# Optimization experiments

Hardware: AMD Instinct MI355X
Metric: run time of the kernel (lower is better)

Reference implementation:

```python
import jax, jax.numpy as jnp
import numpy as np

D_MODEL = 1024
NUM_HEADS = 16
DEPTH = D_MODEL // NUM_HEADS


def setup_inputs() -> dict:
    key = jax.random.key(0)
    ks = jax.random.split(key, 11)
    B, S = 2, 2048
    scale = 1.0 / np.sqrt(D_MODEL)
    inp = {
        "q": jax.random.normal(ks[0], (B, S, D_MODEL), dtype=jnp.float32),
        "k": jax.random.normal(ks[1], (B, S, D_MODEL), dtype=jnp.float32),
        "v": jax.random.normal(ks[2], (B, S, D_MODEL), dtype=jnp.float32),
        "mask": jnp.zeros((B, 1, 1, S), dtype=jnp.float32),
        "wq": jax.random.normal(ks[3], (D_MODEL, D_MODEL), dtype=jnp.float32) * scale,
        "bq": jnp.zeros((D_MODEL,), dtype=jnp.float32),
        "wk": jax.random.normal(ks[4], (D_MODEL, D_MODEL), dtype=jnp.float32) * scale,
        "bk": jnp.zeros((D_MODEL,), dtype=jnp.float32),
        "wv": jax.random.normal(ks[5], (D_MODEL, D_MODEL), dtype=jnp.float32) * scale,
        "bv": jnp.zeros((D_MODEL,), dtype=jnp.float32),
        "wo": jax.random.normal(ks[6], (D_MODEL, D_MODEL), dtype=jnp.float32) * scale,
        "bo": jnp.zeros((D_MODEL,), dtype=jnp.float32),
    }
    return inp


def _split_heads(x):
    # [B, S, D] -> [B, H, S, depth]
    B, S, _ = x.shape
    return x.reshape(B, S, NUM_HEADS, DEPTH).transpose(0, 2, 1, 3)


def reference(q, k, v, mask, wq, bq, wk, bk, wv, bv, wo, bo):
    B, S, _ = q.shape
    qh = _split_heads(q @ wq + bq)  # [B,H,S,d]
    kh = _split_heads(k @ wk + bk)
    vh = _split_heads(v @ wv + bv)
    logits = jnp.einsum("bhsd,bhtd->bhst", qh, kh) / jnp.sqrt(
        jnp.asarray(DEPTH, dtype=qh.dtype)
    )
    logits = logits + mask * -1e9
    attn = jax.nn.softmax(logits, axis=-1)  # [B,H,S,S]
    ctx = jnp.einsum("bhst,bhtd->bhsd", attn, vh)
    ctx = ctx.transpose(0, 2, 1, 3).reshape(B, S, D_MODEL)
    out = ctx @ wo + bo
    return out, attn
```

## Files before the change

kernel.cpp:

```cpp
#include <hip/hip_runtime.h>
#include <cstdint>
#include <cstddef>

typedef __bf16 bf16;
typedef __attribute__((ext_vector_type(8))) __bf16 bf16x8;
typedef __attribute__((ext_vector_type(4))) __bf16 bf16x4;
typedef __attribute__((ext_vector_type(4))) float f32x4;

#define DM 1024
#define NH 16
#define DEPTH 64
#define SEQ 2048
#define NB 2

__device__ __forceinline__ void split2(float x, bf16& h, bf16& l) {
    h = (bf16)x;
    l = (bf16)(x - (float)h);
}

__device__ __forceinline__ f32x4 mfma16(bf16x8 a, bf16x8 b, f32x4 c) {
    return __builtin_amdgcn_mfma_f32_16x16x32_bf16(a, b, c, 0, 0, 0);
}

__global__ __launch_bounds__(256) void split_kernel(const float* __restrict__ x,
                                                    bf16* __restrict__ hi,
                                                    bf16* __restrict__ lo, int n) {
    int i = (blockIdx.x * 256 + threadIdx.x) * 4;
    if (i >= n) return;
    float4 v = *(const float4*)(x + i);
    bf16 h0, l0, h1, l1, h2, l2, h3, l3;
    split2(v.x, h0, l0); split2(v.y, h1, l1);
    split2(v.z, h2, l2); split2(v.w, h3, l3);
    bf16x4 hv = {h0, h1, h2, h3}, lv = {l0, l1, l2, l3};
    *(bf16x4*)(hi + i) = hv;
    *(bf16x4*)(lo + i) = lv;
}

__global__ __launch_bounds__(256) void wsplit_t(const float* __restrict__ w,
                                                bf16* __restrict__ hi,
                                                bf16* __restrict__ lo) {
    __shared__ float tile[64][65];
    int t = threadIdx.x;
    int c0 = blockIdx.x * 64;
    int r0 = blockIdx.y * 64;
    int r = t >> 2, cg = (t & 3) * 16;
#pragma unroll
    for (int j = 0; j < 16; j += 4) {
        float4 v = *(const float4*)(w + (size_t)(r0 + r) * DM + c0 + cg + j);
        tile[r][cg + j] = v.x; tile[r][cg + j + 1] = v.y;
        tile[r][cg + j + 2] = v.z; tile[r][cg + j + 3] = v.w;
    }
    __syncthreads();
    int n = t >> 2, kg = (t & 3) * 16;
    bf16x8 hv0, hv1, lv0, lv1;
#pragma unroll
    for (int i = 0; i < 8; i++) {
        bf16 h, l;
        split2(tile[kg + i][n], h, l); hv0[i] = h; lv0[i] = l;
        split2(tile[kg + 8 + i][n], h, l); hv1[i] = h; lv1[i] = l;
    }
    size_t o = (size_t)(c0 + n) * DM + r0 + kg;
    *(bf16x8*)(hi + o) = hv0; *(bf16x8*)(hi + o + 8) = hv1;
    *(bf16x8*)(lo + o) = lv0; *(bf16x8*)(lo + o + 8) = lv1;
}

__global__ __launch_bounds__(256) void gemm_split(
    const bf16* __restrict__ Ah, const bf16* __restrict__ Al,
    const bf16* __restrict__ Bh, const bf16* __restrict__ Bl,
    const float* __restrict__ bias,
    bf16* __restrict__ Ch, bf16* __restrict__ Cl, float* __restrict__ Cf) {
    __shared__ bf16 lAh[128][40], lAl[128][40], lBh[128][40], lBl[128][40];
    int t = threadIdx.x;
    int m0 = blockIdx.x * 128, n0 = blockIdx.y * 128;
    int l = t & 63, w = t >> 6;
    int quad = l >> 4, ln = l & 15;
    int mr = (w & 1) * 64, nr = (w >> 1) * 64;

    f32x4 acc[4][4];
#pragma unroll
    for (int r = 0; r < 4; r++)
#pragma unroll
        for (int c = 0; c < 4; c++) acc[r][c] = (f32x4){0.f, 0.f, 0.f, 0.f};

    int srow = t >> 1, shalf = (t & 1) * 16;
    for (int kk = 0; kk < DM / 32; kk++) {
        int k0 = kk * 32;
        size_t ga = (size_t)(m0 + srow) * DM + k0 + shalf;
        size_t gb = (size_t)(n0 + srow) * DM + k0 + shalf;
        *(bf16x8*)&lAh[srow][shalf]     = *(const bf16x8*)(Ah + ga);
        *(bf16x8*)&lAh[srow][shalf + 8] = *(const bf16x8*)(Ah + ga + 8);
        *(bf16x8*)&lAl[srow][shalf]     = *(const bf16x8*)(Al + ga);
        *(bf16x8*)&lAl[srow][shalf + 8] = *(const bf16x8*)(Al + ga + 8);
        *(bf16x8*)&lBh[srow][shalf]     = *(const bf16x8*)(Bh + gb);
        *(bf16x8*)&lBh[srow][shalf + 8] = *(const bf16x8*)(Bh + gb + 8);
        *(bf16x8*)&lBl[srow][shalf]     = *(const bf16x8*)(Bl + gb);
        *(bf16x8*)&lBl[srow][shalf + 8] = *(const bf16x8*)(Bl + gb + 8);
        __syncthreads();

        bf16x8 af_h[4], af_l[4], bf_h[4], bf_l[4];
#pragma unroll
        for (int r = 0; r < 4; r++) {
            af_h[r] = *(const bf16x8*)&lAh[mr + r * 16 + ln][quad * 8];
            af_l[r] = *(const bf16x8*)&lAl[mr + r * 16 + ln][quad * 8];
        }
#pragma unroll
        for (int c = 0; c < 4; c++) {
            bf_h[c] = *(const bf16x8*)&lBh[nr + c * 16 + ln][quad * 8];
            bf_l[c] = *(const bf16x8*)&lBl[nr + c * 16 + ln][quad * 8];
        }
#pragma unroll
        for (int r = 0; r < 4; r++)
#pragma unroll
            for (int c = 0; c < 4; c++) {
                acc[r][c] = mfma16(af_h[r], bf_h[c], acc[r][c]);
                acc[r][c] = mfma16(af_h[r], bf_l[c], acc[r][c]);
                acc[r][c] = mfma16(af_l[r], bf_h[c], acc[r][c]);
            }
        __syncthreads();
    }

#pragma unroll
    for (int c = 0; c < 4; c++) {
        int col = n0 + nr + c * 16 + ln;
        float bv = bias[col];
#pragma unroll
        for (int r = 0; r < 4; r++) {
            int rowb = m0 + mr + r * 16 + quad * 4;
#pragma unroll
            for (int i = 0; i < 4; i++) {
                float v = acc[r][c][i] + bv;
                size_t o = (size_t)(rowb + i) * DM + col;
                if (Cf) {
                    Cf[o] = v;
                } else {
                    bf16 h, lo_;
                    split2(v, h, lo_);
                    Ch[o] = h; Cl[o] = lo_;
                }
            }
        }
    }
}

__global__ __launch_bounds__(256) void vtrans(const bf16* __restrict__ vh_h,
                                              const bf16* __restrict__ vh_l,
                                              bf16* __restrict__ vt_h,
                                              bf16* __restrict__ vt_l) {
    __shared__ bf16 tile[64][72];
    int t = threadIdx.x;
    int s0 = blockIdx.x * 64;
    int bh = blockIdx.y;
    int b = bh >> 4, h = bh & 15;
    const bf16* src[2] = {vh_h, vh_l};
    bf16* dst[2] = {vt_h, vt_l};
#pragma unroll
    for (int p = 0; p < 2; p++) {
#pragma unroll
        for (int rnd = 0; rnd < 2; rnd++) {
            int unit = t + rnd * 256;
            int r = unit >> 3, cg = (unit & 7) * 8;
            *(bf16x8*)&tile[r][cg] =
                *(const bf16x8*)(src[p] + (size_t)(b * SEQ + s0 + r) * DM + h * DEPTH + cg);
        }
        __syncthreads();
#pragma unroll
        for (int rnd = 0; rnd < 2; rnd++) {
            int unit = t + rnd * 256;
            int d = unit >> 3, sg = (unit & 7) * 8;
            bf16x8 v;
#pragma unroll
            for (int j = 0; j < 8; j++) v[j] = tile[sg + j][d];
            *(bf16x8*)(dst[p] + (size_t)(bh * DEPTH + d) * SEQ + s0 + sg) = v;
        }
        __syncthreads();
    }
}

__global__ __launch_bounds__(256) void attn_kernel(
    const bf16* __restrict__ qh_h, const bf16* __restrict__ qh_l,
    const bf16* __restrict__ kh_h, const bf16* __restrict__ kh_l,
    const bf16* __restrict__ vt_h, const bf16* __restrict__ vt_l,
    const float* __restrict__ mask,
    float* __restrict__ attn, bf16* __restrict__ ctx_h, bf16* __restrict__ ctx_l) {
    __shared__ bf16 lQh[64][72], lQl[64][72], lKh[64][72], lKl[64][72];
    __shared__ bf16 lVh[64][72], lVl[64][72], lPh[64][72], lPl[64][72];
    int t = threadIdx.x;
    int m0 = blockIdx.x * 64;
    int bh = blockIdx.y;
    int b = bh >> 4, h = bh & 15;
    int l = t & 63, w = t >> 6, quad = l >> 4, ln = l & 15;
    int mr = w * 16;

#pragma unroll
    for (int rnd = 0; rnd < 2; rnd++) {
        int unit = t + rnd * 256;
        int r = unit >> 3, cg = (unit & 7) * 8;
        size_t g = (size_t)(b * SEQ + m0 + r) * DM + h * DEPTH + cg;
        *(bf16x8*)&lQh[r][cg] = *(const bf16x8*)(qh_h + g);
        *(bf16x8*)&lQl[r][cg] = *(const bf16x8*)(qh_l + g);
    }
    __syncthreads();
    bf16x8 qf_h[2], qf_l[2];
#pragma unroll
    for (int kk = 0; kk < 2; kk++) {
        qf_h[kk] = *(const bf16x8*)&lQh[mr + ln][kk * 32 + quad * 8];
        qf_l[kk] = *(const bf16x8*)&lQl[mr + ln][kk * 32 + quad * 8];
    }

    float rowsum[4] = {0.f, 0.f, 0.f, 0.f};
    for (int ct = 0; ct < SEQ / 64; ct++) {
        int t0 = ct * 64;
#pragma unroll
        for (int rnd = 0; rnd < 2; rnd++) {
            int unit = t + rnd * 256;
            int r = unit >> 3, cg = (unit & 7) * 8;
            size_t g = (size_t)(b * SEQ + t0 + r) * DM + h * DEPTH + cg;
            *(bf16x8*)&lKh[r][cg] = *(const bf16x8*)(kh_h + g);
            *(bf16x8*)&lKl[r][cg] = *(const bf16x8*)(kh_l + g);
        }
        __syncthreads();
#pragma unroll
        for (int c = 0; c < 4; c++) {
            f32x4 s = (f32x4){0.f, 0.f, 0.f, 0.f};
#pragma unroll
            for (int kk = 0; kk < 2; kk++) {
                bf16x8 kb_h = *(const bf16x8*)&lKh[c * 16 + ln][kk * 32 + quad * 8];
                bf16x8 kb_l = *(const bf16x8*)&lKl[c * 16 + ln][kk * 32 + quad * 8];
                s = mfma16(qf_h[kk], kb_h, s);
                s = mfma16(qf_h[kk], kb_l, s);
                s = mfma16(qf_l[kk], kb_h, s);
            }
            int col = t0 + c * 16 + ln;
            float mv = mask[b * SEQ + col] * -1e9f;
#pragma unroll
            for (int i = 0; i < 4; i++) rowsum[i] += __expf(s[i] * 0.125f + mv);
        }
        __syncthreads();
    }
#pragma unroll
    for (int m = 1; m < 16; m <<= 1)
#pragma unroll
        for (int i = 0; i < 4; i++) rowsum[i] += __shfl_xor(rowsum[i], m, 64);
    float linv[4];
#pragma unroll
    for (int i = 0; i < 4; i++) linv[i] = 1.0f / rowsum[i];

    f32x4 o[4];
#pragma unroll
    for (int c = 0; c < 4; c++) o[c] = (f32x4){0.f, 0.f, 0.f, 0.f};

    for (int ct = 0; ct < SEQ / 64; ct++) {
        int t0 = ct * 64;
#pragma unroll
        for (int rnd = 0; rnd < 2; rnd++) {
            int unit = t + rnd * 256;
            int r = unit >> 3, cg = (unit & 7) * 8;
            size_t g = (size_t)(b * SEQ + t0 + r) * DM + h * DEPTH + cg;
            *(bf16x8*)&lKh[r][cg] = *(const bf16x8*)(kh_h + g);
            *(bf16x8*)&lKl[r][cg] = *(const bf16x8*)(kh_l + g);
            size_t gv = (size_t)(bh * DEPTH + r) * SEQ + t0 + cg;
            *(bf16x8*)&lVh[r][cg] = *(const bf16x8*)(vt_h + gv);
            *(bf16x8*)&lVl[r][cg] = *(const bf16x8*)(vt_l + gv);
        }
        __syncthreads();
#pragma unroll
        for (int c = 0; c < 4; c++) {
            f32x4 s = (f32x4){0.f, 0.f, 0.f, 0.f};
#pragma unroll
            for (int kk = 0; kk < 2; kk++) {
                bf16x8 kb_h = *(const bf16x8*)&lKh[c * 16 + ln][kk * 32 + quad * 8];
                bf16x8 kb_l = *(const bf16x8*)&lKl[c * 16 + ln][kk * 32 + quad * 8];
                s = mfma16(qf_h[kk], kb_h, s);
                s = mfma16(qf_h[kk], kb_l, s);
                s = mfma16(qf_l[kk], kb_h, s);
            }
            int col = t0 + c * 16 + ln;
            float mv = mask[b * SEQ + col] * -1e9f;
#pragma unroll
            for (int i = 0; i < 4; i++) {
                float p = __expf(s[i] * 0.125f + mv) * linv[i];
                attn[((size_t)bh * SEQ + m0 + mr + quad * 4 + i) * SEQ + col] = p;
                bf16 ph, pl;
                split2(p, ph, pl);
                lPh[mr + quad * 4 + i][c * 16 + ln] = ph;
                lPl[mr + quad * 4 + i][c * 16 + ln] = pl;
            }
        }
        __syncthreads();
#pragma unroll
        for (int kk = 0; kk < 2; kk++) {
            bf16x8 pa_h = *(const bf16x8*)&lPh[mr + ln][kk * 32 + quad * 8];
            bf16x8 pa_l = *(const bf16x8*)&lPl[mr + ln][kk * 32 + quad * 8];
#pragma unroll
            for (int c2 = 0; c2 < 4; c2++) {
                bf16x8 vb_h = *(const bf16x8*)&lVh[c2 * 16 + ln][kk * 32 + quad * 8];
                bf16x8 vb_l = *(const bf16x8*)&lVl[c2 * 16 + ln][kk * 32 + quad * 8];
                o[c2] = mfma16(pa_h, vb_h, o[c2]);
                o[c2] = mfma16(pa_h, vb_l, o[c2]);
                o[c2] = mfma16(pa_l, vb_h, o[c2]);
            }
        }
        __syncthreads();
    }

#pragma unroll
    for (int c2 = 0; c2 < 4; c2++) {
        int d = c2 * 16 + ln;
#pragma unroll
        for (int i = 0; i < 4; i++) {
            int row = m0 + mr + quad * 4 + i;
            bf16 hh, ll;
            split2(o[c2][i], hh, ll);
            size_t oo = (size_t)(b * SEQ + row) * DM + h * DEPTH + d;
            ctx_h[oo] = hh; ctx_l[oo] = ll;
        }
    }
}

extern "C" void kernel_launch(void* const* d_in, const int* in_sizes, int n_in,
                              void* d_out, int out_size, void* d_ws, size_t ws_size,
                              hipStream_t stream) {
    (void)in_sizes; (void)n_in; (void)out_size; (void)ws_size;
    const float* q    = (const float*)d_in[0];
    const float* k    = (const float*)d_in[1];
    const float* v    = (const float*)d_in[2];
    const float* mask = (const float*)d_in[3];
    const float* wq   = (const float*)d_in[4];
    const float* bq   = (const float*)d_in[5];
    const float* wk   = (const float*)d_in[6];
    const float* bk   = (const float*)d_in[7];
    const float* wv   = (const float*)d_in[8];
    const float* bv   = (const float*)d_in[9];
    const float* wo   = (const float*)d_in[10];
    const float* bo   = (const float*)d_in[11];

    float* out  = (float*)d_out;
    float* attn = out + (size_t)NB * SEQ * DM;

    const size_t E  = (size_t)NB * SEQ * DM;
    const size_t WE = (size_t)DM * DM;

    bf16* p = (bf16*)d_ws;
    bf16* q_h = p;            bf16* q_l = q_h + E;
    bf16* k_h = q_l + E;      bf16* k_l = k_h + E;
    bf16* v_h = k_l + E;      bf16* v_l = v_h + E;
    bf16* wqT_h = v_l + E;    bf16* wqT_l = wqT_h + WE;
    bf16* wkT_h = wqT_l + WE; bf16* wkT_l = wkT_h + WE;
    bf16* wvT_h = wkT_l + WE; bf16* wvT_l = wvT_h + WE;
    bf16* woT_h = wvT_l + WE; bf16* woT_l = woT_h + WE;
    bf16* qh_h = woT_l + WE;  bf16* qh_l = qh_h + E;
    bf16* kh_h = qh_l + E;    bf16* kh_l = kh_h + E;
    bf16* vh_h = kh_l + E;    bf16* vh_l = vh_h + E;
    bf16* vt_h = q_h;  bf16* vt_l = q_l;
    bf16* ctx_h = k_h; bf16* ctx_l = k_l;

    dim3 blk(256);
    split_kernel<<<(int)(E / 1024), blk, 0, stream>>>(q, q_h, q_l, (int)E);
    split_kernel<<<(int)(E / 1024), blk, 0, stream>>>(k, k_h, k_l, (int)E);
    split_kernel<<<(int)(E / 1024), blk, 0, stream>>>(v, v_h, v_l, (int)E);
    wsplit_t<<<dim3(16, 16), blk, 0, stream>>>(wq, wqT_h, wqT_l);
    wsplit_t<<<dim3(16, 16), blk, 0, stream>>>(wk, wkT_h, wkT_l);
    wsplit_t<<<dim3(16, 16), blk, 0, stream>>>(wv, wvT_h, wvT_l);
    wsplit_t<<<dim3(16, 16), blk, 0, stream>>>(wo, woT_h, woT_l);

    gemm_split<<<dim3(32, 8), blk, 0, stream>>>(q_h, q_l, wqT_h, wqT_l, bq, qh_h, qh_l, nullptr);
    gemm_split<<<dim3(32, 8), blk, 0, stream>>>(k_h, k_l, wkT_h, wkT_l, bk, kh_h, kh_l, nullptr);
    gemm_split<<<dim3(32, 8), blk, 0, stream>>>(v_h, v_l, wvT_h, wvT_l, bv, vh_h, vh_l, nullptr);

    vtrans<<<dim3(32, 32), blk, 0, stream>>>(vh_h, vh_l, vt_h, vt_l);

    attn_kernel<<<dim3(32, 32), blk, 0, stream>>>(qh_h, qh_l, kh_h, kh_l, vt_h, vt_l,
                                                  mask, attn, ctx_h, ctx_l);

    gemm_split<<<dim3(32, 8), blk, 0, stream>>>(ctx_h, ctx_l, woT_h, woT_l, bo,
                                                nullptr, nullptr, out);
}
```

Before: 1.031 ms.

## Double-buffer GEMM and attention tiles with direct global-to-LDS loads and swizzling

```diff
diff --git a/kernel.cpp b/kernel.cpp
--- a/kernel.cpp
+++ b/kernel.cpp
@@ -20,6 +20,12 @@
 
 __device__ __forceinline__ f32x4 mfma16(bf16x8 a, bf16x8 b, f32x4 c) {
     return __builtin_amdgcn_mfma_f32_16x16x32_bf16(a, b, c, 0, 0, 0);
+}
+
+__device__ __forceinline__ void gload16(const bf16* g, bf16* s) {
+    __builtin_amdgcn_global_load_lds(
+        (const __attribute__((address_space(1))) void*)g,
+        (__attribute__((address_space(3))) void*)s, 16, 0, 0);
 }
 
 __global__ __launch_bounds__(256) void split_kernel(const float* __restrict__ x,
@@ -64,68 +70,82 @@
     *(bf16x8*)(lo + o) = lv0; *(bf16x8*)(lo + o + 8) = lv1;
 }
 
-__global__ __launch_bounds__(256) void gemm_split(
+__global__ __launch_bounds__(512) void gemm_split(
     const bf16* __restrict__ Ah, const bf16* __restrict__ Al,
     const bf16* __restrict__ Bh, const bf16* __restrict__ Bl,
     const float* __restrict__ bias,
     bf16* __restrict__ Ch, bf16* __restrict__ Cl, float* __restrict__ Cf) {
-    __shared__ bf16 lAh[128][40], lAl[128][40], lBh[128][40], lBl[128][40];
+    __shared__ bf16 lds4[2][4][128 * 64];
     int t = threadIdx.x;
     int m0 = blockIdx.x * 128, n0 = blockIdx.y * 128;
     int l = t & 63, w = t >> 6;
     int quad = l >> 4, ln = l & 15;
-    int mr = (w & 1) * 64, nr = (w >> 1) * 64;
-
-    f32x4 acc[4][4];
+    int wr = w >> 2, wc = w & 3;
+    int rch = l >> 3, c16 = l & 7;
+    int sx0 = (quad ^ (ln & 7)) << 3;
+
+    int bufid = w >> 1;
+    const bf16* src = (bufid == 0) ? Ah : (bufid == 1) ? Al : (bufid == 2) ? Bh : Bl;
+    int rbase = (bufid < 2) ? m0 : n0;
+    int ch0 = (w & 1) * 8;
+
+    auto stage = [&](int db, int k0) {
+#pragma unroll
+        for (int j = 0; j < 8; j++) {
+            int chunk = ch0 + j;
+            int row = chunk * 8 + rch;
+            gload16(src + (size_t)(rbase + row) * DM + k0 + ((c16 ^ (row & 7)) << 3),
+                    &lds4[db][bufid][chunk * 512]);
+        }
+    };
+
+    f32x4 acc[4][2];
 #pragma unroll
     for (int r = 0; r < 4; r++)
 #pragma unroll
-        for (int c = 0; c < 4; c++) acc[r][c] = (f32x4){0.f, 0.f, 0.f, 0.f};
-
-    int srow = t >> 1, shalf = (t & 1) * 16;
-    for (int kk = 0; kk < DM / 32; kk++) {
-        int k0 = kk * 32;
-        size_t ga = (size_t)(m0 + srow) * DM + k0 + shalf;
-        size_t gb = (size_t)(n0 + srow) * DM + k0 + shalf;
-        *(bf16x8*)&lAh[srow][shalf]     = *(const bf16x8*)(Ah + ga);
-        *(bf16x8*)&lAh[srow][shalf + 8] = *(const bf16x8*)(Ah + ga + 8);
-        *(bf16x8*)&lAl[srow][shalf]     = *(const bf16x8*)(Al + ga);
-        *(bf16x8*)&lAl[srow][shalf + 8] = *(const bf16x8*)(Al + ga + 8);
-        *(bf16x8*)&lBh[srow][shalf]     = *(const bf16x8*)(Bh + gb);
-        *(bf16x8*)&lBh[srow][shalf + 8] = *(const bf16x8*)(Bh + gb + 8);
-        *(bf16x8*)&lBl[srow][shalf]     = *(const bf16x8*)(Bl + gb);
-        *(bf16x8*)&lBl[srow][shalf + 8] = *(const bf16x8*)(Bl + gb + 8);
+        for (int c = 0; c < 2; c++) acc[r][c] = (f32x4){0.f, 0.f, 0.f, 0.f};
+
+    stage(0, 0);
+    __syncthreads();
+
+    for (int kk = 0; kk < DM / 64; kk++) {
+        int cur = kk & 1;
+        if (kk < DM / 64 - 1) stage(cur ^ 1, (kk + 1) * 64);
+#pragma unroll
+        for (int k2 = 0; k2 < 2; k2++) {
+            int so = sx0 ^ (k2 << 5);
+            bf16x8 ah[4], al[4], bh[2], bl[2];
+#pragma unroll
+            for (int r = 0; r < 4; r++) {
+                int ro = (wr * 64 + r * 16 + ln) << 6;
+                ah[r] = *(const bf16x8*)&lds4[cur][0][ro + so];
+                al[r] = *(const bf16x8*)&lds4[cur][1][ro + so];
+            }
+#pragma unroll
+            for (int c = 0; c < 2; c++) {
+                int ro = (wc * 32 + c * 16 + ln) << 6;
+                bh[c] = *(const bf16x8*)&lds4[cur][2][ro + so];
+                bl[c] = *(const bf16x8*)&lds4[cur][3][ro + so];
+            }
+#pragma unroll
+            for (int r = 0; r < 4; r++)
+#pragma unroll
+                for (int c = 0; c < 2; c++) {
+                    acc[r][c] = mfma16(ah[r], bh[c], acc[r][c]);
+                    acc[r][c] = mfma16(ah[r], bl[c], acc[r][c]);
+                    acc[r][c] = mfma16(al[r], bh[c], acc[r][c]);
+                }
+        }
         __syncthreads();
-
-        bf16x8 af_h[4], af_l[4], bf_h[4], bf_l[4];
+    }
+
+#pragma unroll
+    for (int c = 0; c < 2; c++) {
+        int col = n0 + wc * 32 + c * 16 + ln;
+        float bv = bias[col];
 #pragma unroll
         for (int r = 0; r < 4; r++) {
-            af_h[r] = *(const bf16x8*)&lAh[mr + r * 16 + ln][quad * 8];
-            af_l[r] = *(const bf16x8*)&lAl[mr + r * 16 + ln][quad * 8];
-        }
-#pragma unroll
-        for (int c = 0; c < 4; c++) {
-            bf_h[c] = *(const bf16x8*)&lBh[nr + c * 16 + ln][quad * 8];
-            bf_l[c] = *(const bf16x8*)&lBl[nr + c * 16 + ln][quad * 8];
-        }
-#pragma unroll
-        for (int r = 0; r < 4; r++)
-#pragma unroll
-            for (int c = 0; c < 4; c++) {
-                acc[r][c] = mfma16(af_h[r], bf_h[c], acc[r][c]);
-                acc[r][c] = mfma16(af_h[r], bf_l[c], acc[r][c]);
-                acc[r][c] = mfma16(af_l[r], bf_h[c], acc[r][c]);
-            }
-        __syncthreads();
-    }
-
-#pragma unroll
-    for (int c = 0; c < 4; c++) {
-        int col = n0 + nr + c * 16 + ln;
-        float bv = bias[col];
-#pragma unroll
-        for (int r = 0; r < 4; r++) {
-            int rowb = m0 + mr + r * 16 + quad * 4;
+            int rowb = m0 + wr * 64 + r * 16 + quad * 4;
 #pragma unroll
             for (int i = 0; i < 4; i++) {
                 float v = acc[r][c][i] + bv;
@@ -176,56 +196,79 @@
     }
 }
 
-__global__ __launch_bounds__(256) void attn_kernel(
+#define PST 76
+__global__ __launch_bounds__(512) void attn_kernel(
     const bf16* __restrict__ qh_h, const bf16* __restrict__ qh_l,
     const bf16* __restrict__ kh_h, const bf16* __restrict__ kh_l,
     const bf16* __restrict__ vt_h, const bf16* __restrict__ vt_l,
     const float* __restrict__ mask,
     float* __restrict__ attn, bf16* __restrict__ ctx_h, bf16* __restrict__ ctx_l) {
-    __shared__ bf16 lQh[64][72], lQl[64][72], lKh[64][72], lKl[64][72];
-    __shared__ bf16 lVh[64][72], lVl[64][72], lPh[64][72], lPl[64][72];
+    __shared__ bf16 lK[2][2][64 * 64];
+    __shared__ bf16 lV[2][2][64 * 64];
+    __shared__ bf16 lPh[128 * PST], lPl[128 * PST];
     int t = threadIdx.x;
-    int m0 = blockIdx.x * 64;
+    int m0 = blockIdx.x * 128;
     int bh = blockIdx.y;
     int b = bh >> 4, h = bh & 15;
     int l = t & 63, w = t >> 6, quad = l >> 4, ln = l & 15;
-    int mr = w * 16;
-
-#pragma unroll
-    for (int rnd = 0; rnd < 2; rnd++) {
-        int unit = t + rnd * 256;
-        int r = unit >> 3, cg = (unit & 7) * 8;
-        size_t g = (size_t)(b * SEQ + m0 + r) * DM + h * DEPTH + cg;
-        *(bf16x8*)&lQh[r][cg] = *(const bf16x8*)(qh_h + g);
-        *(bf16x8*)&lQl[r][cg] = *(const bf16x8*)(qh_l + g);
-    }
+    int rch = l >> 3, c16 = l & 7;
+    int sx0 = (quad ^ (ln & 7)) << 3;
+
+    bf16x8 qf_h[2], qf_l[2];
+    {
+        size_t qrow = (size_t)(b * SEQ + m0 + w * 16 + ln) * DM + h * DEPTH;
+#pragma unroll
+        for (int kk = 0; kk < 2; kk++) {
+            qf_h[kk] = *(const bf16x8*)(qh_h + qrow + kk * 32 + quad * 8);
+            qf_l[kk] = *(const bf16x8*)(qh_l + qrow + kk * 32 + quad * 8);
+        }
+    }
+
+    const bf16* ksrc1 = (w < 4) ? kh_h : kh_l;
+    int kbuf1 = (w < 4) ? 0 : 1;
+    int kch0 = (w & 3) * 2;
+    auto stageK = [&](int db, int t0) {
+#pragma unroll
+        for (int j = 0; j < 2; j++) {
+            int chunk = kch0 + j;
+            int row = chunk * 8 + rch;
+            gload16(ksrc1 + (size_t)(b * SEQ + t0 + row) * DM + h * DEPTH +
+                        ((c16 ^ (row & 7)) << 3),
+                    &lK[db][kbuf1][chunk * 512]);
+        }
+    };
+    int tgt = w >> 1;
+    const bf16* ksrc2 = (tgt == 0) ? kh_h : (tgt == 1) ? kh_l : (tgt == 2) ? vt_h : vt_l;
+    auto stageKV = [&](int db, int t0) {
+        bf16* dst = (tgt == 0) ? &lK[db][0][0] : (tgt == 1) ? &lK[db][1][0]
+                  : (tgt == 2) ? &lV[db][0][0] : &lV[db][1][0];
+#pragma unroll
+        for (int j = 0; j < 4; j++) {
+            int chunk = (w & 1) * 4 + j;
+            int row = chunk * 8 + rch;
+            size_t off = (tgt >= 2)
+                             ? ((size_t)(bh * DEPTH + row) * SEQ + t0)
+                             : ((size_t)(b * SEQ + t0 + row) * DM + h * DEPTH);
+            gload16(ksrc2 + off + ((c16 ^ (row & 7)) << 3), dst + chunk * 512);
+        }
+    };
+
+    float rowsum[4] = {0.f, 0.f, 0.f, 0.f};
+    stageK(0, 0);
     __syncthreads();
-    bf16x8 qf_h[2], qf_l[2];
-#pragma unroll
-    for (int kk = 0; kk < 2; kk++) {
-        qf_h[kk] = *(const bf16x8*)&lQh[mr + ln][kk * 32 + quad * 8];
-        qf_l[kk] = *(const bf16x8*)&lQl[mr + ln][kk * 32 + quad * 8];
-    }
-
-    float rowsum[4] = {0.f, 0.f, 0.f, 0.f};
     for (int ct = 0; ct < SEQ / 64; ct++) {
+        int db = ct & 1;
+        if (ct < SEQ / 64 - 1) stageK(db ^ 1, (ct + 1) * 64);
         int t0 = ct * 64;
-#pragma unroll
-        for (int rnd = 0; rnd < 2; rnd++) {
-            int unit = t + rnd * 256;
-            int r = unit >> 3, cg = (unit & 7) * 8;
-            size_t g = (size_t)(b * SEQ + t0 + r) * DM + h * DEPTH + cg;
-            *(bf16x8*)&lKh[r][cg] = *(const bf16x8*)(kh_h + g);
-            *(bf16x8*)&lKl[r][cg] = *(const bf16x8*)(kh_l + g);
-        }
-        __syncthreads();
 #pragma unroll
         for (int c = 0; c < 4; c++) {
             f32x4 s = (f32x4){0.f, 0.f, 0.f, 0.f};
 #pragma unroll
             for (int kk = 0; kk < 2; kk++) {
-                bf16x8 kb_h = *(const bf16x8*)&lKh[c * 16 + ln][kk * 32 + quad * 8];
-                bf16x8 kb_l = *(const bf16x8*)&lKl[c * 16 + ln][kk * 32 + quad * 8];
+                int so = sx0 ^ (kk << 5);
+                int ro = (c * 16 + ln) << 6;
+                bf16x8 kb_h = *(const bf16x8*)&lK[db][0][ro + so];
+                bf16x8 kb_l = *(const bf16x8*)&lK[db][1][ro + so];
                 s = mfma16(qf_h[kk], kb_h, s);
                 s = mfma16(qf_h[kk], kb_l, s);
                 s = mfma16(qf_l[kk], kb_h, s);
@@ -247,29 +290,23 @@
 
     f32x4 o[4];
 #pragma unroll
-    for (int c = 0; c < 4; c++) o[c] = (f32x4){0.f, 0.f, 0.f, 0.f};
-
+    for (int c2 = 0; c2 < 4; c2++) o[c2] = (f32x4){0.f, 0.f, 0.f, 0.f};
+
+    stageKV(0, 0);
+    __syncthreads();
     for (int ct = 0; ct < SEQ / 64; ct++) {
+        int db = ct & 1;
+        if (ct < SEQ / 64 - 1) stageKV(db ^ 1, (ct + 1) * 64);
         int t0 = ct * 64;
-#pragma unroll
-        for (int rnd = 0; rnd < 2; rnd++) {
-            int unit = t + rnd * 256;
-            int r = unit >> 3, cg = (unit & 7) * 8;
-            size_t g = (size_t)(b * SEQ + t0 + r) * DM + h * DEPTH + cg;
-            *(bf16x8*)&lKh[r][cg] = *(const bf16x8*)(kh_h + g);
-            *(bf16x8*)&lKl[r][cg] = *(const bf16x8*)(kh_l + g);
-            size_t gv = (size_t)(bh * DEPTH + r) * SEQ + t0 + cg;
-            *(bf16x8*)&lVh[r][cg] = *(const bf16x8*)(vt_h + gv);
-            *(bf16x8*)&lVl[r][cg] = *(const bf16x8*)(vt_l + gv);
-        }
-        __syncthreads();
 #pragma unroll
         for (int c = 0; c < 4; c++) {
             f32x4 s = (f32x4){0.f, 0.f, 0.f, 0.f};
 #pragma unroll
             for (int kk = 0; kk < 2; kk++) {
-                bf16x8 kb_h = *(const bf16x8*)&lKh[c * 16 + ln][kk * 32 + quad * 8];
-                bf16x8 kb_l = *(const bf16x8*)&lKl[c * 16 + ln][kk * 32 + quad * 8];
+                int so = sx0 ^ (kk << 5);
+                int ro = (c * 16 + ln) << 6;
+                bf16x8 kb_h = *(const bf16x8*)&lK[db][0][ro + so];
+                bf16x8 kb_l = *(const bf16x8*)&lK[db][1][ro + so];
                 s = mfma16(qf_h[kk], kb_h, s);
                 s = mfma16(qf_h[kk], kb_l, s);
                 s = mfma16(qf_l[kk], kb_h, s);
@@ -279,22 +316,25 @@
 #pragma unroll
             for (int i = 0; i < 4; i++) {
                 float p = __expf(s[i] * 0.125f + mv) * linv[i];
-                attn[((size_t)bh * SEQ + m0 + mr + quad * 4 + i) * SEQ + col] = p;
+                __builtin_nontemporal_store(
+                    p, attn + ((size_t)bh * SEQ + m0 + w * 16 + quad * 4 + i) * SEQ + col);
                 bf16 ph, pl;
                 split2(p, ph, pl);
-                lPh[mr + quad * 4 + i][c * 16 + ln] = ph;
-                lPl[mr + quad * 4 + i][c * 16 + ln] = pl;
-            }
-        }
-        __syncthreads();
+                int pr = (w * 16 + quad * 4 + i) * PST + c * 16 + ln;
+                lPh[pr] = ph;
+                lPl[pr] = pl;
+            }
+        }
 #pragma unroll
         for (int kk = 0; kk < 2; kk++) {
-            bf16x8 pa_h = *(const bf16x8*)&lPh[mr + ln][kk * 32 + quad * 8];
-            bf16x8 pa_l = *(const bf16x8*)&lPl[mr + ln][kk * 32 + quad * 8];
+            int so = sx0 ^ (kk << 5);
+            bf16x8 pa_h = *(const bf16x8*)&lPh[(w * 16 + ln) * PST + kk * 32 + quad * 8];
+            bf16x8 pa_l = *(const bf16x8*)&lPl[(w * 16 + ln) * PST + kk * 32 + quad * 8];
 #pragma unroll
             for (int c2 = 0; c2 < 4; c2++) {
-                bf16x8 vb_h = *(const bf16x8*)&lVh[c2 * 16 + ln][kk * 32 + quad * 8];
-                bf16x8 vb_l = *(const bf16x8*)&lVl[c2 * 16 + ln][kk * 32 + quad * 8];
+                int ro = (c2 * 16 + ln) << 6;
+                bf16x8 vb_h = *(const bf16x8*)&lV[db][0][ro + so];
+                bf16x8 vb_l = *(const bf16x8*)&lV[db][1][ro + so];
                 o[c2] = mfma16(pa_h, vb_h, o[c2]);
                 o[c2] = mfma16(pa_h, vb_l, o[c2]);
                 o[c2] = mfma16(pa_l, vb_h, o[c2]);
@@ -308,7 +348,7 @@
         int d = c2 * 16 + ln;
 #pragma unroll
         for (int i = 0; i < 4; i++) {
-            int row = m0 + mr + quad * 4 + i;
+            int row = m0 + w * 16 + quad * 4 + i;
             bf16 hh, ll;
             split2(o[c2][i], hh, ll);
             size_t oo = (size_t)(b * SEQ + row) * DM + h * DEPTH + d;
@@ -363,15 +403,15 @@
     wsplit_t<<<dim3(16, 16), blk, 0, stream>>>(wv, wvT_h, wvT_l);
     wsplit_t<<<dim3(16, 16), blk, 0, stream>>>(wo, woT_h, woT_l);
 
-    gemm_split<<<dim3(32, 8), blk, 0, stream>>>(q_h, q_l, wqT_h, wqT_l, bq, qh_h, qh_l, nullptr);
-    gemm_split<<<dim3(32, 8), blk, 0, stream>>>(k_h, k_l, wkT_h, wkT_l, bk, kh_h, kh_l, nullptr);
-    gemm_split<<<dim3(32, 8), blk, 0, stream>>>(v_h, v_l, wvT_h, wvT_l, bv, vh_h, vh_l, nullptr);
+    gemm_split<<<dim3(32, 8), dim3(512), 0, stream>>>(q_h, q_l, wqT_h, wqT_l, bq, qh_h, qh_l, nullptr);
+    gemm_split<<<dim3(32, 8), dim3(512), 0, stream>>>(k_h, k_l, wkT_h, wkT_l, bk, kh_h, kh_l, nullptr);
+    gemm_split<<<dim3(32, 8), dim3(512), 0, stream>>>(v_h, v_l, wvT_h, wvT_l, bv, vh_h, vh_l, nullptr);
 
     vtrans<<<dim3(32, 32), blk, 0, stream>>>(vh_h, vh_l, vt_h, vt_l);
 
-    attn_kernel<<<dim3(32, 32), blk, 0, stream>>>(qh_h, qh_l, kh_h, kh_l, vt_h, vt_l,
-                                                  mask, attn, ctx_h, ctx_l);
-
-    gemm_split<<<dim3(32, 8), blk, 0, stream>>>(ctx_h, ctx_l, woT_h, woT_l, bo,
-                                                nullptr, nullptr, out);
-}
+    attn_kernel<<<dim3(16, 32), dim3(512), 0, stream>>>(qh_h, qh_l, kh_h, kh_l, vt_h, vt_l,
+                                                        mask, attn, ctx_h, ctx_l);
+
+    gemm_split<<<dim3(32, 8), dim3(512), 0, stream>>>(ctx_h, ctx_l, woT_h, woT_l, bo,
+                                                      nullptr, nullptr, out);
+}
```

New measurement: 898.8 us. 1.15x faster.
